# Performance work log

Hardware: AMD Instinct MI355X
Metric: run time of the kernel (lower is better)

The kernel has to match this reference:

```python
import jax, jax.numpy as jnp
import numpy as np

B, S, D_MODEL, H = 2, 2048, 1024, 16
DIMS = D_MODEL // H  # 64


def setup_inputs() -> dict:
    key = jax.random.key(0)
    ks = jax.random.split(key, 7)
    scale = 1.0 / np.sqrt(D_MODEL)
    x = jax.random.normal(ks[0], (B, S, D_MODEL), dtype=jnp.float32)
    # Stacked per-head projection params: nn.Linear(d_model, dims) per head
    Wq = jax.random.uniform(ks[1], (H, DIMS, D_MODEL), minval=-scale, maxval=scale, dtype=jnp.float32)
    Wk = jax.random.uniform(ks[2], (H, DIMS, D_MODEL), minval=-scale, maxval=scale, dtype=jnp.float32)
    Wv = jax.random.uniform(ks[3], (H, DIMS, D_MODEL), minval=-scale, maxval=scale, dtype=jnp.float32)
    bq = jax.random.uniform(ks[4], (H, DIMS), minval=-scale, maxval=scale, dtype=jnp.float32)
    bk = jax.random.uniform(ks[5], (H, DIMS), minval=-scale, maxval=scale, dtype=jnp.float32)
    bv = jax.random.uniform(ks[6], (H, DIMS), minval=-scale, maxval=scale, dtype=jnp.float32)
    return {"x": x, "Wq": Wq, "Wk": Wk, "Wv": Wv, "bq": bq, "bk": bk, "bv": bv}


def reference(x, Wq, Wk, Wv, bq, bk, bv):
    # Per-head linear projections: [B,S,D] x [H,E,D] -> [B,H,S,E]
    q = jnp.einsum('bsd,hed->bhse', x, Wq) + bq[None, :, None, :]
    k = jnp.einsum('bsd,hed->bhse', x, Wk) + bk[None, :, None, :]
    v = jnp.einsum('bsd,hed->bhse', x, Wv) + bv[None, :, None, :]
    norm = DIMS ** (-0.5)
    # (q @ k^T) * norm @ v  -- NO softmax, as in the source
    scores = jnp.einsum('bhse,bhte->bhst', q, k) * norm  # [B,H,S,S]
    out = jnp.einsum('bhst,bhte->bhse', scores, v)       # [B,H,S,E]
    # concat heads along feature dim (head order matches torch.cat)
    return out.transpose(0, 2, 1, 3).reshape(B, S, H * DIMS)
```

## Files before the change

kernel.cpp:

```cpp
#include <hip/hip_runtime.h>


typedef __attribute__((ext_vector_type(8))) __bf16 bf16x8;
typedef __attribute__((ext_vector_type(8))) short short8;
typedef __attribute__((ext_vector_type(4))) float f32x4;

#define NX  4194304
#define NW1 1048576
#define NW  3145728

__device__ __forceinline__ float bf2f(unsigned short u) {
  union { unsigned int i; float f; } v; v.i = ((unsigned int)u) << 16; return v.f;
}
__device__ __forceinline__ unsigned short f2bf(float f) {
  union { float f; unsigned int i; } v; v.f = f;
  unsigned int u = v.i;
  u += 0x7fffu + ((u >> 16) & 1u);
  return (unsigned short)(u >> 16);
}

__device__ __forceinline__ void gload_lds16(const void* g, void* l) {
  __builtin_amdgcn_global_load_lds(
      (const __attribute__((address_space(1))) void*)(unsigned long long)(g),
      (__attribute__((address_space(3))) void*)(unsigned int)(unsigned long long)(l),
      16, 0, 0);
}

__global__ __launch_bounds__(256) void convert_pack(
    const float* __restrict__ x,
    const float* __restrict__ wq, const float* __restrict__ wk,
    const float* __restrict__ wv,
    const float* __restrict__ bq, const float* __restrict__ bk,
    const float* __restrict__ bv,
    unsigned short* __restrict__ Xbf, unsigned short* __restrict__ Wcat,
    float* __restrict__ Bcat)
{
  const long long t8 = ((long long)blockIdx.x * 256 + threadIdx.x) * 8;
  const float* src;
  unsigned short* dst;
  long long off;
  if (t8 < NX) {
    src = x; dst = Xbf; off = t8;
  } else if (t8 < NX + NW) {
    const long long w = t8 - NX;
    const int z = (int)(w >> 20);
    off = w & (NW1 - 1);
    src = (z == 0) ? wq : (z == 1) ? wk : wv;
    dst = Wcat + (long long)z * NW1;
  } else if (t8 < NX + NW + 3072) {
    const long long bo = t8 - (NX + NW);
    const int z = (int)(bo >> 10);
    const long long o2 = bo & 1023;
    const float* bsrc = (z == 0) ? bq : (z == 1) ? bk : bv;
    *(f32x4*)(Bcat + z * 1024 + o2)     = *(const f32x4*)(bsrc + o2);
    *(f32x4*)(Bcat + z * 1024 + o2 + 4) = *(const f32x4*)(bsrc + o2 + 4);
    return;
  } else {
    return;
  }
  f32x4 v0 = *(const f32x4*)(src + off);
  f32x4 v1 = *(const f32x4*)(src + off + 4);
  union { short8 s; unsigned short u[8]; } o;
#pragma unroll
  for (int j = 0; j < 4; ++j) {
    o.u[j]     = f2bf(v0[j]);
    o.u[4 + j] = f2bf(v1[j]);
  }
  *(short8*)(dst + off) = o.s;
}

__global__ __launch_bounds__(256, 2) void qkv_gemm(
    const unsigned short* __restrict__ Xbf,
    const unsigned short* __restrict__ Wcat,
    const float* __restrict__ Bcat,
    unsigned short* __restrict__ QKV)
{
  __shared__ unsigned short smA[128 * 64];
  __shared__ unsigned short smB[128 * 64];

  const int tid = threadIdx.x;
  int bid = blockIdx.x;
  bid = (bid & 7) * 96 + (bid >> 3);
  const int colBase = (bid % 24) * 128;
  const int rowBase = (bid / 24) * 128;

  const int lane = tid & 63;
  const int wid  = tid >> 6;
  const int wr = (wid >> 1) * 64;
  const int wc = (wid & 1) * 64;
  const int lr = lane & 15;
  const int lk = lane >> 4;

  f32x4 acc[4][4] = {};

  for (int kt = 0; kt < 16; ++kt) {
    const int k0 = kt * 64;
#pragma unroll
    for (int i = 0; i < 4; ++i) {
      const int si = i * 256 + tid;
      const int row = si >> 3, seg = si & 7;
      const int sseg = seg ^ (row & 7);
      gload_lds16(Xbf  + (size_t)(rowBase + row) * 1024 + k0 + sseg * 8,
                  smA + (si & ~63) * 8);
      gload_lds16(Wcat + (size_t)(colBase + row) * 1024 + k0 + sseg * 8,
                  smB + (si & ~63) * 8);
    }
    __syncthreads();

#pragma unroll
    for (int ks = 0; ks < 2; ++ks) {
      bf16x8 av[4], bv4[4];
#pragma unroll
      for (int m = 0; m < 4; ++m) {
        const int row = wr + m * 16 + lr;
        av[m] = *(const bf16x8*)((const char*)smA + row * 128 +
                                 (((ks * 4 + lk) ^ (row & 7)) * 16));
      }
#pragma unroll
      for (int n = 0; n < 4; ++n) {
        const int row = wc + n * 16 + lr;
        bv4[n] = *(const bf16x8*)((const char*)smB + row * 128 +
                                  (((ks * 4 + lk) ^ (row & 7)) * 16));
      }
#pragma unroll
      for (int m = 0; m < 4; ++m)
#pragma unroll
        for (int n = 0; n < 4; ++n)
          acc[m][n] = __builtin_amdgcn_mfma_f32_16x16x32_bf16(av[m], bv4[n], acc[m][n], 0, 0, 0);
    }
    __syncthreads();
  }

  float bvals[4];
#pragma unroll
  for (int n = 0; n < 4; ++n)
    bvals[n] = Bcat[colBase + wc + n * 16 + lr];
#pragma unroll
  for (int m = 0; m < 4; ++m) {
#pragma unroll
    for (int j = 0; j < 4; ++j) {
      const int row = rowBase + wr + m * 16 + lk * 4 + j;
#pragma unroll
      for (int n = 0; n < 4; ++n) {
        const int col = colBase + wc + n * 16 + lr;
        QKV[(size_t)row * 3072 + col] = f2bf(acc[m][n][j] + bvals[n]);
      }
    }
  }
}

__global__ __launch_bounds__(256) void kv_outer(
    const unsigned short* __restrict__ QKV, float* __restrict__ Mpart)
{
  __shared__ float Ks[64 * 64];
  __shared__ float Vs[64 * 64];
  const int tid = threadIdx.x;
  const int blk = blockIdx.x;
  const int bh = blk >> 3, ch = blk & 7;
  const int b = bh >> 4, h = bh & 15;
  const int f0 = (tid & 15) * 4;
  const int e0 = (tid >> 4) * 4;
  float acc[4][4] = {};
  const size_t base = ((size_t)b * 2048 + ch * 256) * 3072 + h * 64;

  for (int c = 0; c < 4; ++c) {
#pragma unroll
    for (int i = 0; i < 2; ++i) {
      const int si = i * 256 + tid;
      const int row = si >> 3, seg = si & 7;
      const size_t g = base + (size_t)(c * 64 + row) * 3072 + seg * 8;
      short8 kr = *(const short8*)&QKV[g + 1024];
      short8 vr = *(const short8*)&QKV[g + 2048];
      f32x4 k0v, k1v, v0v, v1v;
#pragma unroll
      for (int j = 0; j < 4; ++j) {
        k0v[j] = bf2f((unsigned short)kr[j]);
        k1v[j] = bf2f((unsigned short)kr[4 + j]);
        v0v[j] = bf2f((unsigned short)vr[j]);
        v1v[j] = bf2f((unsigned short)vr[4 + j]);
      }
      *(f32x4*)&Ks[row * 64 + seg * 8]     = k0v;
      *(f32x4*)&Ks[row * 64 + seg * 8 + 4] = k1v;
      *(f32x4*)&Vs[row * 64 + seg * 8]     = v0v;
      *(f32x4*)&Vs[row * 64 + seg * 8 + 4] = v1v;
    }
    __syncthreads();
#pragma unroll 4
    for (int tt = 0; tt < 64; ++tt) {
      f32x4 kf = *(const f32x4*)&Ks[tt * 64 + f0];
      f32x4 vf = *(const f32x4*)&Vs[tt * 64 + e0];
#pragma unroll
      for (int i2 = 0; i2 < 4; ++i2)
#pragma unroll
        for (int j2 = 0; j2 < 4; ++j2)
          acc[i2][j2] += kf[i2] * vf[j2];
    }
    __syncthreads();
  }
  float* out = Mpart + (size_t)blk * 4096;
#pragma unroll
  for (int i2 = 0; i2 < 4; ++i2) {
    f32x4 o = { acc[i2][0], acc[i2][1], acc[i2][2], acc[i2][3] };
    *(f32x4*)&out[(f0 + i2) * 64 + e0] = o;
  }
}

__global__ __launch_bounds__(256) void m_reduce(
    const float* __restrict__ Mpart, float* __restrict__ M)
{
  const int bh = blockIdx.x;
  const int tid = threadIdx.x;
#pragma unroll
  for (int i = 0; i < 4; ++i) {
    const int off = i * 1024 + tid * 4;
    f32x4 s = {};
#pragma unroll
    for (int ch = 0; ch < 8; ++ch)
      s += *(const f32x4*)&Mpart[((size_t)bh * 8 + ch) * 4096 + off];
    s *= 0.125f;
    *(f32x4*)&M[(size_t)bh * 4096 + off] = s;
  }
}

__global__ __launch_bounds__(256) void qm_out(
    const unsigned short* __restrict__ QKV, const float* __restrict__ M,
    float* __restrict__ Out)
{
  __shared__ float Ms[64 * 64];
  __shared__ float Qs[128 * 65];
  const int tid = threadIdx.x;
  const int b = blockIdx.z, h = blockIdx.y, s0 = blockIdx.x * 128;
  const int bh = b * 16 + h;

#pragma unroll
  for (int i = 0; i < 4; ++i) {
    const int off = i * 1024 + tid * 4;
    *(f32x4*)&Ms[off] = *(const f32x4*)&M[(size_t)bh * 4096 + off];
  }
  const size_t qbase = ((size_t)b * 2048 + s0) * 3072 + h * 64;
#pragma unroll
  for (int i = 0; i < 4; ++i) {
    const int si = i * 256 + tid;
    const int row = si >> 3, seg = si & 7;
    short8 q = *(const short8*)&QKV[qbase + (size_t)row * 3072 + seg * 8];
#pragma unroll
    for (int j = 0; j < 8; ++j)
      Qs[row * 65 + seg * 8 + j] = bf2f((unsigned short)q[j]);
  }
  __syncthreads();

  const int s = (tid >> 3) * 4;
  const int e0 = (tid & 7) * 8;
  float acc2[4][8] = {};
  for (int f = 0; f < 64; ++f) {
    f32x4 m0 = *(const f32x4*)&Ms[f * 64 + e0];
    f32x4 m1 = *(const f32x4*)&Ms[f * 64 + e0 + 4];
#pragma unroll
    for (int i = 0; i < 4; ++i) {
      const float q = Qs[(s + i) * 65 + f];
#pragma unroll
      for (int j = 0; j < 4; ++j) {
        acc2[i][j]     += q * m0[j];
        acc2[i][j + 4] += q * m1[j];
      }
    }
  }
  const size_t obase = ((size_t)b * 2048 + s0) * 1024 + h * 64;
#pragma unroll
  for (int i = 0; i < 4; ++i) {
    f32x4 o0 = { acc2[i][0], acc2[i][1], acc2[i][2], acc2[i][3] };
    f32x4 o1 = { acc2[i][4], acc2[i][5], acc2[i][6], acc2[i][7] };
    *(f32x4*)&Out[obase + (size_t)(s + i) * 1024 + e0]     = o0;
    *(f32x4*)&Out[obase + (size_t)(s + i) * 1024 + e0 + 4] = o1;
  }
}

extern "C" void kernel_launch(void* const* d_in, const int* in_sizes, int n_in,
                              void* d_out, int out_size, void* d_ws, size_t ws_size,
                              hipStream_t stream) {
  const float* x  = (const float*)d_in[0];
  const float* Wq = (const float*)d_in[1];
  const float* Wk = (const float*)d_in[2];
  const float* Wv = (const float*)d_in[3];
  const float* bq = (const float*)d_in[4];
  const float* bk = (const float*)d_in[5];
  const float* bv = (const float*)d_in[6];
  float* out = (float*)d_out;

  char* ws = (char*)d_ws;
  const size_t MiB = 1024ull * 1024ull;
  unsigned short* Xbf   = (unsigned short*)(ws);
  unsigned short* Wcat  = (unsigned short*)(ws + 8  * MiB);
  float*          Bcat  = (float*)         (ws + 14 * MiB);
  unsigned short* QKV   = (unsigned short*)(ws + 15 * MiB);
  float*          Mpart = (float*)         (ws + 39 * MiB);
  float*          Mfin  = (float*)         (ws + 43 * MiB);

  convert_pack<<<3586, 256, 0, stream>>>(x, Wq, Wk, Wv, bq, bk, bv,
                                         Xbf, Wcat, Bcat);
  qkv_gemm<<<768, 256, 0, stream>>>(Xbf, Wcat, Bcat, QKV);
  kv_outer<<<256, 256, 0, stream>>>(QKV, Mpart);
  m_reduce<<<32, 256, 0, stream>>>(Mpart, Mfin);
  qm_out<<<dim3(16, 16, 2), 256, 0, stream>>>(QKV, Mfin, out);
}
```

Measured before the change: 70.77 us.

## Store Q/K/V transposed per head and compute K^T V with MFMA

The QKV GEMM epilogue now writes Q, K and V into separate per-head transposed buffers laid out [b,h,feature,seq], with 4-element packed stores. kv_outer uses that layout to load K and V fragments straight from global memory into bf16 MFMA instructions, one wave per block, in place of the fp32 LDS outer-product loop. qm_out reads the transposed Q tile into LDS. This removes the scalar FMA work and the LDS staging in kv_outer, but the GEMM epilogue stores become strided across features and the MFMA kernel runs only 64-thread blocks.

```diff
diff --git a/kernel.cpp b/kernel.cpp
--- a/kernel.cpp
+++ b/kernel.cpp
@@ -4,6 +4,7 @@
 typedef __attribute__((ext_vector_type(8))) __bf16 bf16x8;
 typedef __attribute__((ext_vector_type(8))) short short8;
 typedef __attribute__((ext_vector_type(4))) float f32x4;
+typedef __attribute__((ext_vector_type(4))) unsigned short ushort4v;
 
 #define NX  4194304
 #define NW1 1048576
@@ -73,7 +74,9 @@
     const unsigned short* __restrict__ Xbf,
     const unsigned short* __restrict__ Wcat,
     const float* __restrict__ Bcat,
-    unsigned short* __restrict__ QKV)
+    unsigned short* __restrict__ Qt,
+    unsigned short* __restrict__ Kt,
+    unsigned short* __restrict__ Vt)
 {
   __shared__ unsigned short smA[128 * 64];
   __shared__ unsigned short smB[128 * 64];
@@ -131,78 +134,64 @@
     __syncthreads();
   }
 
-  float bvals[4];
-#pragma unroll
-  for (int n = 0; n < 4; ++n)
-    bvals[n] = Bcat[colBase + wc + n * 16 + lr];
-#pragma unroll
-  for (int m = 0; m < 4; ++m) {
-#pragma unroll
-    for (int j = 0; j < 4; ++j) {
-      const int row = rowBase + wr + m * 16 + lk * 4 + j;
-#pragma unroll
-      for (int n = 0; n < 4; ++n) {
-        const int col = colBase + wc + n * 16 + lr;
-        QKV[(size_t)row * 3072 + col] = f2bf(acc[m][n][j] + bvals[n]);
-      }
-    }
-  }
-}
-
-__global__ __launch_bounds__(256) void kv_outer(
-    const unsigned short* __restrict__ QKV, float* __restrict__ Mpart)
-{
-  __shared__ float Ks[64 * 64];
-  __shared__ float Vs[64 * 64];
-  const int tid = threadIdx.x;
+  const int zone = colBase >> 10;
+  unsigned short* __restrict__ T = (zone == 0) ? Qt : (zone == 1) ? Kt : Vt;
+  const int bB = rowBase >> 11;
+#pragma unroll
+  for (int n = 0; n < 4; ++n) {
+    const int colG = colBase + wc + n * 16 + lr;
+    const float bval = Bcat[colG];
+    const int hf = (colG >> 6) & 15;
+    const int f  = colG & 63;
+    const size_t rowOff = ((size_t)(bB * 16 + hf) * 64 + f) * 2048;
+#pragma unroll
+    for (int m = 0; m < 4; ++m) {
+      const int t = (rowBase + wr + m * 16 + lk * 4) & 2047;
+      ushort4v pk;
+#pragma unroll
+      for (int j = 0; j < 4; ++j)
+        pk[j] = f2bf(acc[m][n][j] + bval);
+      *(ushort4v*)&T[rowOff + t] = pk;
+    }
+  }
+}
+
+__global__ __launch_bounds__(64) void kv_outer(
+    const unsigned short* __restrict__ Kt,
+    const unsigned short* __restrict__ Vt,
+    float* __restrict__ Mpart)
+{
+  const int lane = threadIdx.x;
   const int blk = blockIdx.x;
-  const int bh = blk >> 3, ch = blk & 7;
-  const int b = bh >> 4, h = bh & 15;
-  const int f0 = (tid & 15) * 4;
-  const int e0 = (tid >> 4) * 4;
-  float acc[4][4] = {};
-  const size_t base = ((size_t)b * 2048 + ch * 256) * 3072 + h * 64;
-
-  for (int c = 0; c < 4; ++c) {
-#pragma unroll
-    for (int i = 0; i < 2; ++i) {
-      const int si = i * 256 + tid;
-      const int row = si >> 3, seg = si & 7;
-      const size_t g = base + (size_t)(c * 64 + row) * 3072 + seg * 8;
-      short8 kr = *(const short8*)&QKV[g + 1024];
-      short8 vr = *(const short8*)&QKV[g + 2048];
-      f32x4 k0v, k1v, v0v, v1v;
-#pragma unroll
-      for (int j = 0; j < 4; ++j) {
-        k0v[j] = bf2f((unsigned short)kr[j]);
-        k1v[j] = bf2f((unsigned short)kr[4 + j]);
-        v0v[j] = bf2f((unsigned short)vr[j]);
-        v1v[j] = bf2f((unsigned short)vr[4 + j]);
-      }
-      *(f32x4*)&Ks[row * 64 + seg * 8]     = k0v;
-      *(f32x4*)&Ks[row * 64 + seg * 8 + 4] = k1v;
-      *(f32x4*)&Vs[row * 64 + seg * 8]     = v0v;
-      *(f32x4*)&Vs[row * 64 + seg * 8 + 4] = v1v;
-    }
-    __syncthreads();
-#pragma unroll 4
-    for (int tt = 0; tt < 64; ++tt) {
-      f32x4 kf = *(const f32x4*)&Ks[tt * 64 + f0];
-      f32x4 vf = *(const f32x4*)&Vs[tt * 64 + e0];
-#pragma unroll
-      for (int i2 = 0; i2 < 4; ++i2)
-#pragma unroll
-        for (int j2 = 0; j2 < 4; ++j2)
-          acc[i2][j2] += kf[i2] * vf[j2];
-    }
-    __syncthreads();
+  const int bh = blk >> 3, tc = blk & 7;
+  const int lr = lane & 15, lk = lane >> 4;
+  const size_t base = (size_t)bh * 64 * 2048;
+
+  f32x4 acc[4][4] = {};
+#pragma unroll
+  for (int ks = 0; ks < 8; ++ks) {
+    const int t0 = tc * 256 + ks * 32 + lk * 8;
+    bf16x8 af[4], bf[4];
+#pragma unroll
+    for (int m = 0; m < 4; ++m)
+      af[m] = *(const bf16x8*)&Kt[base + (size_t)(m * 16 + lr) * 2048 + t0];
+#pragma unroll
+    for (int n = 0; n < 4; ++n)
+      bf[n] = *(const bf16x8*)&Vt[base + (size_t)(n * 16 + lr) * 2048 + t0];
+#pragma unroll
+    for (int m = 0; m < 4; ++m)
+#pragma unroll
+      for (int n = 0; n < 4; ++n)
+        acc[m][n] = __builtin_amdgcn_mfma_f32_16x16x32_bf16(af[m], bf[n], acc[m][n], 0, 0, 0);
   }
   float* out = Mpart + (size_t)blk * 4096;
 #pragma unroll
-  for (int i2 = 0; i2 < 4; ++i2) {
-    f32x4 o = { acc[i2][0], acc[i2][1], acc[i2][2], acc[i2][3] };
-    *(f32x4*)&out[(f0 + i2) * 64 + e0] = o;
-  }
+  for (int m = 0; m < 4; ++m)
+#pragma unroll
+    for (int n = 0; n < 4; ++n)
+#pragma unroll
+      for (int j = 0; j < 4; ++j)
+        out[(m * 16 + lk * 4 + j) * 64 + n * 16 + lr] = acc[m][n][j];
 }
 
 __global__ __launch_bounds__(256) void m_reduce(
@@ -223,11 +212,11 @@
 }
 
 __global__ __launch_bounds__(256) void qm_out(
-    const unsigned short* __restrict__ QKV, const float* __restrict__ M,
+    const unsigned short* __restrict__ Qt, const float* __restrict__ M,
     float* __restrict__ Out)
 {
   __shared__ float Ms[64 * 64];
-  __shared__ float Qs[128 * 65];
+  __shared__ float Qst[64 * 132];
   const int tid = threadIdx.x;
   const int b = blockIdx.z, h = blockIdx.y, s0 = blockIdx.x * 128;
   const int bh = b * 16 + h;
@@ -237,15 +226,15 @@
     const int off = i * 1024 + tid * 4;
     *(f32x4*)&Ms[off] = *(const f32x4*)&M[(size_t)bh * 4096 + off];
   }
-  const size_t qbase = ((size_t)b * 2048 + s0) * 3072 + h * 64;
-#pragma unroll
-  for (int i = 0; i < 4; ++i) {
-    const int si = i * 256 + tid;
-    const int row = si >> 3, seg = si & 7;
-    short8 q = *(const short8*)&QKV[qbase + (size_t)row * 3072 + seg * 8];
+  const size_t qbase = (size_t)bh * 64 * 2048;
+#pragma unroll
+  for (int i = 0; i < 4; ++i) {
+    const int slot = i * 256 + tid;
+    const int f = slot >> 4, c = slot & 15;
+    short8 q = *(const short8*)&Qt[qbase + (size_t)f * 2048 + s0 + c * 8];
 #pragma unroll
     for (int j = 0; j < 8; ++j)
-      Qs[row * 65 + seg * 8 + j] = bf2f((unsigned short)q[j]);
+      Qst[f * 132 + c * 8 + j] = bf2f((unsigned short)q[j]);
   }
   __syncthreads();
 
@@ -257,7 +246,7 @@
     f32x4 m1 = *(const f32x4*)&Ms[f * 64 + e0 + 4];
 #pragma unroll
     for (int i = 0; i < 4; ++i) {
-      const float q = Qs[(s + i) * 65 + f];
+      const float q = Qst[f * 132 + s + i];
 #pragma unroll
       for (int j = 0; j < 4; ++j) {
         acc2[i][j]     += q * m0[j];
@@ -292,14 +281,16 @@
   unsigned short* Xbf   = (unsigned short*)(ws);
   unsigned short* Wcat  = (unsigned short*)(ws + 8  * MiB);
   float*          Bcat  = (float*)         (ws + 14 * MiB);
-  unsigned short* QKV   = (unsigned short*)(ws + 15 * MiB);
+  unsigned short* Qt    = (unsigned short*)(ws + 15 * MiB);
+  unsigned short* Kt    = (unsigned short*)(ws + 23 * MiB);
+  unsigned short* Vt    = (unsigned short*)(ws + 31 * MiB);
   float*          Mpart = (float*)         (ws + 39 * MiB);
   float*          Mfin  = (float*)         (ws + 43 * MiB);
 
   convert_pack<<<3586, 256, 0, stream>>>(x, Wq, Wk, Wv, bq, bk, bv,
                                          Xbf, Wcat, Bcat);
-  qkv_gemm<<<768, 256, 0, stream>>>(Xbf, Wcat, Bcat, QKV);
-  kv_outer<<<256, 256, 0, stream>>>(QKV, Mpart);
+  qkv_gemm<<<768, 256, 0, stream>>>(Xbf, Wcat, Bcat, Qt, Kt, Vt);
+  kv_outer<<<256, 64, 0, stream>>>(Kt, Vt, Mpart);
   m_reduce<<<32, 256, 0, stream>>>(Mpart, Mfin);
-  qm_out<<<dim3(16, 16, 2), 256, 0, stream>>>(QKV, Mfin, out);
-}
+  qm_out<<<dim3(16, 16, 2), 256, 0, stream>>>(Qt, Mfin, out);
+}
```

Result: faster. 65.36 us (-7.6%).
